# Kernel tuning notes

Measured on AMD Instinct MI355X. Metric: run time of the kernel, lower is better.

Reference implementation:

```python
import jax, jax.numpy as jnp
import numpy as np
from jax import lax

RIVER_LENGTH = 50000.0
NUM_SEGMENTS = 20
DT = 3600.0
DX = RIVER_LENGTH / NUM_SEGMENTS
CFL = min(2.0 * DT / DX, 0.9)  # c=2.0 hard-coded in original; clipped to 0.9


def setup_inputs() -> dict:
    key = jax.random.key(0)
    ks = jax.random.split(key, 5)
    B, T = 8192, 4096
    return {
        "runoff": jax.random.uniform(ks[0], (B, T), dtype=jnp.float32) * 10.0,  # mm/hr
        "basin_area": jax.random.uniform(ks[1], (B, 1), dtype=jnp.float32) * 1000.0 + 10.0,  # km^2
        "manning_n": jax.random.uniform(ks[2], (B, 1), dtype=jnp.float32) * 0.05 + 0.01,
        "slope": jax.random.uniform(ks[3], (B, 1), dtype=jnp.float32) * 0.01 + 1e-4,
        "width": jax.random.uniform(ks[4], (B, 1), dtype=jnp.float32) * 50.0 + 1.0,
    }


def reference(runoff, basin_area, manning_n, slope, width):
    # lateral inflow per segment: mm/hr -> m^3/s over basin area, split into segments
    area_m2 = basin_area * 1e6  # (B,1)
    q_lateral = runoff / 1000.0 / 3600.0 * area_m2 / float(NUM_SEGMENTS)  # (B,T)

    B = runoff.shape[0]
    Q0 = jnp.zeros((B, NUM_SEGMENTS + 1), dtype=runoff.dtype)

    def step(Q, q_in):
        # upwind update for segments 1..N using OLD state (matches tf version)
        q_in = q_in[:, None]  # (B,1)
        Q_upd = jnp.maximum(Q[:, 1:] - CFL * (Q[:, 1:] - Q[:, :-1]) + q_in * DT, 0.0)
        Q_new = jnp.concatenate([Q[:, :1], Q_upd], axis=1)  # segment 0 unchanged (stays 0)
        return Q_new, Q_new[:, -1]

    _, outlet = lax.scan(step, Q0, q_lateral.T)  # outlet: (T,B)
    return outlet.T  # (B,T) discharge in m^3/s
```

## Files before the change

### kernel.cpp

```cpp
#include <hip/hip_runtime.h>


#define KTAIL  6
#define HALO   32
#define RPT    16
#define TPB    256
#define TILE_T (TPB * RPT)
#define NQ     ((TILE_T + HALO) / 4)

struct WTail { float w[KTAIL]; };

__device__ __forceinline__ int swz(int q) { return q ^ ((q >> 3) & 7); }

__global__ __launch_bounds__(TPB) void kwr_slide_kernel(
    const float* __restrict__ runoff,
    const float* __restrict__ basin_area,
    float* __restrict__ out,
    int T, int tiles_per_row, WTail wt)
{
    __shared__ float4 lds[NQ];

    const int tid  = threadIdx.x;
    const int b    = blockIdx.x / tiles_per_row;
    const int tile = blockIdx.x - b * tiles_per_row;
    const long long rowbase = (long long)b * T;
    const int tstart = tile * TILE_T - HALO;

    const float4* gsrc = (const float4*)(runoff + rowbase + tstart);
    #pragma unroll
    for (int pass = 0; pass < (NQ + TPB - 1) / TPB; ++pass) {
        int q = tid + pass * TPB;
        if (q < NQ) {
            float4 v = (tstart + 4 * q >= 0) ? gsrc[q]
                                             : make_float4(0.f, 0.f, 0.f, 0.f);
            lds[swz(q)] = v;
        }
    }
    __syncthreads();

    float buf[RPT + HALO];
    #pragma unroll
    for (int c = 0; c < (RPT + HALO) / 4; ++c) {
        float4 v = lds[swz(4 * tid + c)];
        buf[4*c+0] = v.x; buf[4*c+1] = v.y;
        buf[4*c+2] = v.z; buf[4*c+3] = v.w;
    }

    float S = 0.0f;
    #pragma unroll
    for (int i = 13; i <= 32; ++i) S += buf[i];

    float res[RPT];
    #pragma unroll
    for (int r = 0; r < RPT; ++r) {
        if (r > 0) S += buf[32 + r] - buf[12 + r];
        float v = S;
        #pragma unroll
        for (int k = 0; k < KTAIL; ++k)
            v = fmaf(wt.w[k], buf[12 + r - k], v);
        res[r] = v;
    }

    const float s = basin_area[b] * 50.0f;
    float* orow = out + rowbase + tile * TILE_T + tid * RPT;
    #pragma unroll
    for (int g = 0; g < RPT / 4; ++g)
        ((float4*)orow)[g] = make_float4(res[4*g+0]*s, res[4*g+1]*s,
                                         res[4*g+2]*s, res[4*g+3]*s);
}

extern "C" void kernel_launch(void* const* d_in, const int* in_sizes, int n_in,
                              void* d_out, int out_size, void* d_ws, size_t ws_size,
                              hipStream_t stream)
{
    const float* runoff     = (const float*)d_in[0];
    const float* basin_area = (const float*)d_in[1];
    float* out = (float*)d_out;

    const int B = in_sizes[1];
    const int T = in_sizes[0] / B;

    WTail wt;
    double Q[21];
    for (int j = 0; j <= 20; ++j) Q[j] = (j >= 1) ? 1.0 : 0.0;
    for (int k = 1; k <= 25; ++k) {
        for (int j = 20; j >= 1; --j) Q[j] = 0.1 * Q[j] + 0.9 * Q[j - 1];
        if (k >= 20) wt.w[k - 20] = (float)Q[20];
    }

    const int tiles_per_row = T / TILE_T;
    const int nblk = B * tiles_per_row;

    kwr_slide_kernel<<<nblk, TPB, 0, stream>>>(runoff, basin_area, out,
                                               T, tiles_per_row, wt);
}
```

Measured before the change: 254.2 us.

## Pipeline consecutive tiles per block with register prefetch and LDS halo reuse

Each block now processes 8 consecutive 2048-sample tiles instead of one 4096-sample tile. The next tile is prefetched into registers while the current one is computed, and the 32-sample halo comes from the previous tile's LDS buffer instead of being re-read from global memory. This targets redundant halo loads and load latency exposed by one-shot blocks. In exchange there are fewer blocks, which reduces parallelism, and a sync per tile; the halo carry depends on the tiles walking rows in order.

```diff
diff --git a/kernel.cpp b/kernel.cpp
--- a/kernel.cpp
+++ b/kernel.cpp
@@ -1,72 +1,87 @@
 #include <hip/hip_runtime.h>
 
 
+#define TILE   2048
+#define NQT    512
+#define NQB    520
+#define TPB    256
 #define KTAIL  6
-#define HALO   32
-#define RPT    16
-#define TPB    256
-#define TILE_T (TPB * RPT)
-#define NQ     ((TILE_T + HALO) / 4)
 
 struct WTail { float w[KTAIL]; };
 
 __device__ __forceinline__ int swz(int q) { return q ^ ((q >> 3) & 7); }
 
-__global__ __launch_bounds__(TPB) void kwr_slide_kernel(
+__global__ __launch_bounds__(TPB) void kwr_pipe_kernel(
     const float* __restrict__ runoff,
     const float* __restrict__ basin_area,
     float* __restrict__ out,
-    int T, int tiles_per_row, WTail wt)
+    int tiles_per_row, int runs, WTail wt)
 {
-    __shared__ float4 lds[NQ];
+    __shared__ float4 lds[2][NQB];
 
-    const int tid  = threadIdx.x;
-    const int b    = blockIdx.x / tiles_per_row;
-    const int tile = blockIdx.x - b * tiles_per_row;
-    const long long rowbase = (long long)b * T;
-    const int tstart = tile * TILE_T - HALO;
+    const int tid = threadIdx.x;
+    const long long g0 = (long long)blockIdx.x * runs;
 
-    const float4* gsrc = (const float4*)(runoff + rowbase + tstart);
-    #pragma unroll
-    for (int pass = 0; pass < (NQ + TPB - 1) / TPB; ++pass) {
-        int q = tid + pass * TPB;
-        if (q < NQ) {
-            float4 v = (tstart + 4 * q >= 0) ? gsrc[q]
-                                             : make_float4(0.f, 0.f, 0.f, 0.f);
-            lds[swz(q)] = v;
-        }
-    }
-    __syncthreads();
+    int row  = (int)(g0 / tiles_per_row);
+    int half = (int)(g0 % tiles_per_row);
 
-    float buf[RPT + HALO];
-    #pragma unroll
-    for (int c = 0; c < (RPT + HALO) / 4; ++c) {
-        float4 v = lds[swz(4 * tid + c)];
-        buf[4*c+0] = v.x; buf[4*c+1] = v.y;
-        buf[4*c+2] = v.z; buf[4*c+3] = v.w;
+    float4 r0, r1;
+    {
+        const float4* src = (const float4*)(runoff + g0 * TILE);
+        r0 = src[tid];
+        r1 = src[TPB + tid];
     }
 
-    float S = 0.0f;
-    #pragma unroll
-    for (int i = 13; i <= 32; ++i) S += buf[i];
+    for (int j = 0; j < runs; ++j) {
+        const long long g = g0 + j;
+        const int cur = j & 1;
 
-    float res[RPT];
-    #pragma unroll
-    for (int r = 0; r < RPT; ++r) {
-        if (r > 0) S += buf[32 + r] - buf[12 + r];
-        float v = S;
+        lds[cur][swz(8 + tid)]       = r0;
+        lds[cur][swz(8 + TPB + tid)] = r1;
+        if (tid < 8) {
+            float4 h = make_float4(0.f, 0.f, 0.f, 0.f);
+            if (half != 0)
+                h = lds[cur ^ 1][swz(NQT + tid)];
+            lds[cur][swz(tid)] = h;
+        }
+        __syncthreads();
+
+        if (j + 1 < runs) {
+            const float4* src = (const float4*)(runoff + (g + 1) * TILE);
+            r0 = src[tid];
+            r1 = src[TPB + tid];
+        }
+
+        float win[40];
         #pragma unroll
-        for (int k = 0; k < KTAIL; ++k)
-            v = fmaf(wt.w[k], buf[12 + r - k], v);
-        res[r] = v;
+        for (int c = 0; c < 10; ++c) {
+            float4 v = lds[cur][swz(2 * tid + c)];
+            win[4*c+0] = v.x; win[4*c+1] = v.y;
+            win[4*c+2] = v.z; win[4*c+3] = v.w;
+        }
+
+        float S = 0.0f;
+        #pragma unroll
+        for (int i = 13; i <= 32; ++i) S += win[i];
+
+        float res[8];
+        #pragma unroll
+        for (int r = 0; r < 8; ++r) {
+            if (r > 0) S += win[32 + r] - win[12 + r];
+            float v = S;
+            #pragma unroll
+            for (int k = 0; k < KTAIL; ++k)
+                v = fmaf(wt.w[k], win[12 + r - k], v);
+            res[r] = v;
+        }
+
+        const float s = basin_area[row] * 50.0f;
+        float* orow = out + g * TILE + tid * 8;
+        ((float4*)orow)[0] = make_float4(res[0]*s, res[1]*s, res[2]*s, res[3]*s);
+        ((float4*)orow)[1] = make_float4(res[4]*s, res[5]*s, res[6]*s, res[7]*s);
+
+        if (++half == tiles_per_row) { half = 0; ++row; }
     }
-
-    const float s = basin_area[b] * 50.0f;
-    float* orow = out + rowbase + tile * TILE_T + tid * RPT;
-    #pragma unroll
-    for (int g = 0; g < RPT / 4; ++g)
-        ((float4*)orow)[g] = make_float4(res[4*g+0]*s, res[4*g+1]*s,
-                                         res[4*g+2]*s, res[4*g+3]*s);
 }
 
 extern "C" void kernel_launch(void* const* d_in, const int* in_sizes, int n_in,
@@ -88,9 +103,11 @@
         if (k >= 20) wt.w[k - 20] = (float)Q[20];
     }
 
-    const int tiles_per_row = T / TILE_T;
-    const int nblk = B * tiles_per_row;
+    const int tiles_per_row = T / TILE;
+    const long long nt = (long long)B * tiles_per_row;
+    const int runs = 8;
+    const int nblk = (int)(nt / runs);
 
-    kwr_slide_kernel<<<nblk, TPB, 0, stream>>>(runoff, basin_area, out,
-                                               T, tiles_per_row, wt);
+    kwr_pipe_kernel<<<nblk, TPB, 0, stream>>>(runoff, basin_area, out,
+                                              tiles_per_row, runs, wt);
 }
```

Result: faster. 243.4 us (-4.2%).
